# Performance work log

Measured on AMD Instinct MI355X. Metric: run time of the kernel, lower is better.

Reference implementation:

```python
import jax, jax.numpy as jnp
import numpy as np

DIM = 512

def setup_inputs() -> dict:
    key = jax.random.key(0)
    kx, kq, kk, kv = jax.random.split(key, 4)
    x = jax.random.normal(kx, (8, 2048, DIM), dtype=jnp.float32)
    # Dense kernels are [in_dim, out_dim], no bias
    Wq = jax.random.normal(kq, (DIM, DIM), dtype=jnp.float32) * (DIM ** -0.5)
    Wk = jax.random.normal(kk, (DIM, DIM), dtype=jnp.float32) * (DIM ** -0.5)
    Wv = jax.random.normal(kv, (DIM, DIM), dtype=jnp.float32) * (DIM ** -0.5)
    return {"x": x, "Wq": Wq, "Wk": Wk, "Wv": Wv}

def reference(x, Wq, Wk, Wv):
    # x: [b, s, d]
    q = jnp.einsum('bsd,de->bse', x, Wq)
    k = jnp.einsum('bsd,de->bse', x, Wk)
    v = jnp.einsum('bsd,de->bse', x, Wv)
    scale = jnp.sqrt(jnp.asarray(DIM, dtype=x.dtype))
    attn = jnp.einsum('bqe,bke->bqk', q, k) / scale  # [b, s, s]
    attn = jax.nn.softmax(attn, axis=-1)
    return jnp.einsum('bqk,bke->bqe', attn, v)  # [b, s, d]
```

## Files before the change

kernel.cpp:

```cpp
#include <hip/hip_runtime.h>
#include <stdint.h>

typedef unsigned short u16;
typedef unsigned int u32;
typedef float floatx4 __attribute__((ext_vector_type(4)));
typedef __bf16 bf16x8 __attribute__((ext_vector_type(8)));
typedef __attribute__((address_space(1))) const u32 gu32;
typedef __attribute__((address_space(3))) u32 lu32;

#define SEQ 2048
#define DIM 512
#define NBATCH 8

#if defined(__has_builtin)
#if __has_builtin(__builtin_amdgcn_cvt_pk_bf16_f32)
#define HAVE_PK_BF16 1
#endif
#endif
#ifndef HAVE_PK_BF16
#define HAVE_PK_BF16 0
#endif

__device__ __forceinline__ u16 f2bf(float f) {
#if HAVE_PK_BF16
  auto p = __builtin_amdgcn_cvt_pk_bf16_f32(f, f);
  union { decltype(p) v; u16 u[2]; } cv; cv.v = p;
  return cv.u[0];
#else
  u32 u = __float_as_uint(f);
  u += 0x7fffu + ((u >> 16) & 1u);
  return (u16)(u >> 16);
#endif
}

__device__ __forceinline__ void stage_tile64(const u16* __restrict__ g, int ld, int k0, u16* lds) {
  const int t = threadIdx.x;
  const int wave = t >> 6, lane = t & 63;
  const int rsub = lane >> 3;
  const int lg = (lane & 7) ^ rsub;
#pragma unroll
  for (int q = 0; q < 4; ++q) {
    const int chunk = wave * 4 + q;
    const int row = chunk * 8 + rsub;
    const u16* gp = g + (size_t)row * ld + k0 + lg * 8;
    u16* lp = lds + chunk * 512 + lane * 8;
    __builtin_amdgcn_global_load_lds((gu32*)gp, (lu32*)lp, 16, 0, 0);
  }
}

__device__ __forceinline__ void gemm_core(const u16* A, const u16* BT, int lda, int ldb, int kdim,
                                          u16* As, u16* Bs, floatx4 acc[4][4]) {
  const int t = threadIdx.x;
  const int wave = t >> 6, lane = t & 63;
  const int wr = (wave >> 1) * 64, wc = (wave & 1) * 64;
  const int l15 = lane & 15, quad = lane >> 4;
  const int swz = l15 & 7;
  for (int k0 = 0; k0 < kdim; k0 += 64) {
    stage_tile64(A, lda, k0, As);
    stage_tile64(BT, ldb, k0, Bs);
    __syncthreads();
#pragma unroll
    for (int ks = 0; ks < 2; ++ks) {
      const int pg = ((ks << 2) + quad) ^ swz;
      bf16x8 af[4], bfr[4];
#pragma unroll
      for (int i = 0; i < 4; ++i) {
        af[i]  = *(const bf16x8*)(As + (wr + i * 16 + l15) * 64 + pg * 8);
        bfr[i] = *(const bf16x8*)(Bs + (wc + i * 16 + l15) * 64 + pg * 8);
      }
#pragma unroll
      for (int mi = 0; mi < 4; ++mi)
#pragma unroll
        for (int ni = 0; ni < 4; ++ni)
          acc[mi][ni] = __builtin_amdgcn_mfma_f32_16x16x32_bf16(af[mi], bfr[ni], acc[mi][ni], 0, 0, 0);
    }
    __syncthreads();
  }
}

__device__ __forceinline__ void zero_acc(floatx4 acc[4][4]) {
#pragma unroll
  for (int i = 0; i < 4; ++i)
#pragma unroll
    for (int j = 0; j < 4; ++j)
      acc[i][j] = (floatx4){0.f, 0.f, 0.f, 0.f};
}

__global__ __launch_bounds__(256) void k_prep(const float* __restrict__ x,
                                              const float* __restrict__ Wq, const float* __restrict__ Wk,
                                              const float* __restrict__ Wv,
                                              u16* __restrict__ xb, u16* __restrict__ wt) {
  __shared__ float tile[64][65];
  const int t = threadIdx.x;
  if (blockIdx.x < 4096) {
    size_t i = ((size_t)blockIdx.x * 256 + t) * 8;
    float4 a = *(const float4*)(x + i);
    float4 b = *(const float4*)(x + i + 4);
    u16 o[8] = {f2bf(a.x), f2bf(a.y), f2bf(a.z), f2bf(a.w),
                f2bf(b.x), f2bf(b.y), f2bf(b.z), f2bf(b.w)};
    *(uint4*)(xb + i) = *(const uint4*)o;
    return;
  }
  const int r = blockIdx.x - 4096;
  const int sec = r >> 6, rem = r & 63;
  const int kb = (rem & 7) * 64, nb0 = (rem >> 3) * 64;
  const float* W = (sec == 0) ? Wq : (sec == 1) ? Wk : Wv;
#pragma unroll
  for (int i = 0; i < 4; ++i) {
    int kr = i * 16 + (t >> 4), nc = (t & 15) * 4;
    float4 v = *(const float4*)&W[(size_t)(kb + kr) * 512 + nb0 + nc];
    tile[kr][nc] = v.x; tile[kr][nc + 1] = v.y; tile[kr][nc + 2] = v.z; tile[kr][nc + 3] = v.w;
  }
  __syncthreads();
#pragma unroll
  for (int i = 0; i < 4; ++i) {
    int nr = i * 16 + (t >> 4), kc = (t & 15) * 4;
    u16 o[4] = {f2bf(tile[kc][nr]), f2bf(tile[kc + 1][nr]), f2bf(tile[kc + 2][nr]), f2bf(tile[kc + 3][nr])};
    *(uint2*)&wt[(size_t)(sec * 512 + nb0 + nr) * 512 + kb + kc] = *(const uint2*)o;
  }
}

__global__ __launch_bounds__(256, 4) void k_qkv(const u16* __restrict__ xb, const u16* __restrict__ wt,
                                                u16* __restrict__ qo, u16* __restrict__ ko,
                                                u16* __restrict__ vt) {
  __shared__ __align__(16) u16 As[128 * 64];
  __shared__ __align__(16) u16 Bs[128 * 64];
  const int m0 = blockIdx.x * 128, n0 = blockIdx.y * 128;
  floatx4 acc[4][4];
  zero_acc(acc);
  gemm_core(xb + (size_t)m0 * DIM, wt + (size_t)n0 * DIM, DIM, DIM, DIM, As, Bs, acc);
  const int t = threadIdx.x, wave = t >> 6, lane = t & 63;
  const int wr = (wave >> 1) * 64, wc = (wave & 1) * 64;
  const int l15 = lane & 15, quad = lane >> 4;
  const int sec = n0 >> 9;
#pragma unroll
  for (int mi = 0; mi < 4; ++mi)
#pragma unroll
    for (int ni = 0; ni < 4; ++ni)
#pragma unroll
      for (int r = 0; r < 4; ++r) {
        int m = m0 + wr + mi * 16 + quad * 4 + r;
        int n = n0 + wc + ni * 16 + l15;
        float v = acc[mi][ni][r];
        int nc = n & 511;
        if (sec == 0) {
          qo[(size_t)m * DIM + nc] = f2bf(v * 0.04419417382415922f);
        } else if (sec == 1) {
          ko[(size_t)m * DIM + nc] = f2bf(v);
        } else {
          int b = m >> 11, s = m & 2047;
          vt[((size_t)(b * DIM + nc)) * SEQ + s] = f2bf(v);
        }
      }
}

__global__ __launch_bounds__(256, 4) void k_scores(const u16* __restrict__ q, const u16* __restrict__ kk,
                                                   u16* __restrict__ sc, float* __restrict__ rowsum,
                                                   int b0) {
  __shared__ __align__(16) u16 As[128 * 64];
  __shared__ __align__(16) u16 Bs[128 * 64];
  const int bz = blockIdx.z, bb = b0 + bz;
  const int xcd = blockIdx.x & 7, j = blockIdx.x >> 3;
  const int m0 = (j & 15) * 128, n0 = (xcd * 2 + (j >> 4)) * 128;
  floatx4 acc[4][4];
  zero_acc(acc);
  gemm_core(q + (size_t)bb * SEQ * DIM + (size_t)m0 * DIM,
            kk + (size_t)bb * SEQ * DIM + (size_t)n0 * DIM, DIM, DIM, DIM, As, Bs, acc);
  u16* C = sc + (size_t)bz * SEQ * SEQ;
  float* rsb = rowsum + (size_t)bb * SEQ;
  const int t = threadIdx.x, wave = t >> 6, lane = t & 63;
  const int wr = (wave >> 1) * 64, wc = (wave & 1) * 64;
  const int l15 = lane & 15, quad = lane >> 4;
#pragma unroll
  for (int mi = 0; mi < 4; ++mi)
#pragma unroll
    for (int r = 0; r < 4; ++r) {
      int m = m0 + wr + mi * 16 + quad * 4 + r;
      float p = 0.f;
      float ev[4];
#pragma unroll
      for (int ni = 0; ni < 4; ++ni) {
        ev[ni] = __expf(acc[mi][ni][r]);
        p += ev[ni];
      }
#pragma unroll
      for (int ni = 0; ni < 4; ++ni) {
        int n = n0 + wc + ni * 16 + l15;
        C[(size_t)m * SEQ + n] = f2bf(ev[ni]);
      }
      p += __shfl_xor(p, 1); p += __shfl_xor(p, 2);
      p += __shfl_xor(p, 4); p += __shfl_xor(p, 8);
      if (l15 == 0) atomicAdd(&rsb[m], p);
    }
}

__global__ __launch_bounds__(256, 4) void k_pv(const u16* __restrict__ sc, const u16* __restrict__ vt,
                                               const float* __restrict__ rowsum,
                                               float* __restrict__ out, int b0) {
  __shared__ __align__(16) u16 As[128 * 64];
  __shared__ __align__(16) u16 Bs[128 * 64];
  const int bz = blockIdx.z, bb = b0 + bz;
  const int xcd = blockIdx.x & 7, j = blockIdx.x >> 3;
  const int m0 = (xcd * 2 + (j & 1)) * 128, n0 = (j >> 1) * 128;
  floatx4 acc[4][4];
  zero_acc(acc);
  gemm_core(sc + (size_t)bz * SEQ * SEQ + (size_t)m0 * SEQ,
            vt + (size_t)bb * DIM * SEQ + (size_t)n0 * SEQ, SEQ, SEQ, SEQ, As, Bs, acc);
  float* C = out + (size_t)bb * SEQ * DIM;
  const float* rsb = rowsum + (size_t)bb * SEQ;
  const int t = threadIdx.x, wave = t >> 6, lane = t & 63;
  const int wr = (wave >> 1) * 64, wc = (wave & 1) * 64;
  const int l15 = lane & 15, quad = lane >> 4;
#pragma unroll
  for (int mi = 0; mi < 4; ++mi)
#pragma unroll
    for (int r = 0; r < 4; ++r) {
      int m = m0 + wr + mi * 16 + quad * 4 + r;
      float inv = 1.0f / rsb[m];
#pragma unroll
      for (int ni = 0; ni < 4; ++ni) {
        int n = n0 + wc + ni * 16 + l15;
        C[(size_t)m * DIM + n] = acc[mi][ni][r] * inv;
      }
    }
}

extern "C" void kernel_launch(void* const* d_in, const int* in_sizes, int n_in,
                              void* d_out, int out_size, void* d_ws, size_t ws_size,
                              hipStream_t stream) {
  const float* x  = (const float*)d_in[0];
  const float* Wq = (const float*)d_in[1];
  const float* Wk = (const float*)d_in[2];
  const float* Wv = (const float*)d_in[3];
  float* out = (float*)d_out;
  char* ws = (char*)d_ws;

  u16* xb   = (u16*)(ws + 0);
  u16* wt   = (u16*)(ws + 16777216);
  u16* qo   = (u16*)(ws + 18350080);
  u16* ko   = (u16*)(ws + 35127296);
  u16* vt   = (u16*)(ws + 51904512);
  float* rs = (float*)(ws + 68681728);
  u16* sc   = (u16*)(ws + 68747264);
  const size_t base_need = 68747264;
  const size_t per_b = (size_t)SEQ * SEQ * 2;
  size_t avail = (ws_size > base_need) ? (ws_size - base_need) : 0;
  int nb = (int)(avail / per_b);
  if (nb < 1) nb = 1;
  if (nb > NBATCH) nb = NBATCH;

  hipMemsetAsync(rs, 0, (size_t)NBATCH * SEQ * sizeof(float), stream);
  k_prep<<<dim3(4288), dim3(256), 0, stream>>>(x, Wq, Wk, Wv, xb, wt);
  k_qkv<<<dim3(128, 12), dim3(256), 0, stream>>>(xb, wt, qo, ko, vt);
  for (int b0 = 0; b0 < NBATCH; b0 += nb) {
    int nbr = (NBATCH - b0 < nb) ? (NBATCH - b0) : nb;
    k_scores<<<dim3(256, 1, nbr), dim3(256), 0, stream>>>(qo, ko, sc, rs, b0);
    k_pv<<<dim3(64, 1, nbr), dim3(256), 0, stream>>>(sc, vt, rs, out, b0);
  }
}
```

Baseline: 216.0 us.

## Replace block-shared GEMM staging with per-wave double-buffered LDS pipeline

Swaps the block-wide staged GEMM core, which needed two __syncthreads per K step, for a per-wave core. Each wave stages its own 64x32 A and B tiles into private LDS buffers, double-buffered and issued two steps ahead, and uses vmcnt waits instead of barriers. Per-block LDS rises to 64KB, so launch bounds drop to 2 blocks per CU. k_qkv is also remapped to a 1D grid with XCD-aware tile ordering. The intent is to overlap global-to-LDS loads with MFMA work and remove block barriers, at the cost of fetching shared A/B rows once per wave and lower occupancy.

```diff
diff --git a/kernel.cpp b/kernel.cpp
--- a/kernel.cpp
+++ b/kernel.cpp
@@ -12,70 +12,62 @@
 #define DIM 512
 #define NBATCH 8
 
-#if defined(__has_builtin)
-#if __has_builtin(__builtin_amdgcn_cvt_pk_bf16_f32)
-#define HAVE_PK_BF16 1
-#endif
-#endif
-#ifndef HAVE_PK_BF16
-#define HAVE_PK_BF16 0
-#endif
-
 __device__ __forceinline__ u16 f2bf(float f) {
-#if HAVE_PK_BF16
-  auto p = __builtin_amdgcn_cvt_pk_bf16_f32(f, f);
-  union { decltype(p) v; u16 u[2]; } cv; cv.v = p;
-  return cv.u[0];
-#else
   u32 u = __float_as_uint(f);
   u += 0x7fffu + ((u >> 16) & 1u);
   return (u16)(u >> 16);
-#endif
-}
-
-__device__ __forceinline__ void stage_tile64(const u16* __restrict__ g, int ld, int k0, u16* lds) {
-  const int t = threadIdx.x;
-  const int wave = t >> 6, lane = t & 63;
-  const int rsub = lane >> 3;
-  const int lg = (lane & 7) ^ rsub;
-#pragma unroll
-  for (int q = 0; q < 4; ++q) {
-    const int chunk = wave * 4 + q;
-    const int row = chunk * 8 + rsub;
-    const u16* gp = g + (size_t)row * ld + k0 + lg * 8;
-    u16* lp = lds + chunk * 512 + lane * 8;
-    __builtin_amdgcn_global_load_lds((gu32*)gp, (lu32*)lp, 16, 0, 0);
-  }
-}
-
-__device__ __forceinline__ void gemm_core(const u16* A, const u16* BT, int lda, int ldb, int kdim,
-                                          u16* As, u16* Bs, floatx4 acc[4][4]) {
-  const int t = threadIdx.x;
-  const int wave = t >> 6, lane = t & 63;
-  const int wr = (wave >> 1) * 64, wc = (wave & 1) * 64;
-  const int l15 = lane & 15, quad = lane >> 4;
-  const int swz = l15 & 7;
-  for (int k0 = 0; k0 < kdim; k0 += 64) {
-    stage_tile64(A, lda, k0, As);
-    stage_tile64(BT, ldb, k0, Bs);
-    __syncthreads();
-#pragma unroll
-    for (int ks = 0; ks < 2; ++ks) {
-      const int pg = ((ks << 2) + quad) ^ swz;
-      bf16x8 af[4], bfr[4];
-#pragma unroll
-      for (int i = 0; i < 4; ++i) {
-        af[i]  = *(const bf16x8*)(As + (wr + i * 16 + l15) * 64 + pg * 8);
-        bfr[i] = *(const bf16x8*)(Bs + (wc + i * 16 + l15) * 64 + pg * 8);
-      }
-#pragma unroll
-      for (int mi = 0; mi < 4; ++mi)
-#pragma unroll
-        for (int ni = 0; ni < 4; ++ni)
-          acc[mi][ni] = __builtin_amdgcn_mfma_f32_16x16x32_bf16(af[mi], bfr[ni], acc[mi][ni], 0, 0, 0);
-    }
-    __syncthreads();
-  }
+}
+
+template<int KDIM>
+__device__ __forceinline__ void gemm_core_p(const u16* __restrict__ Ah, const u16* __restrict__ Bh,
+                                            int lda, int ldb, u16* __restrict__ wbuf,
+                                            floatx4 acc[4][4]) {
+  const int lane = threadIdx.x & 63;
+  const int l15 = lane & 15, quad = lane >> 4;
+  const int rsub = lane >> 2;
+  const int lg = (lane & 3) ^ ((rsub >> 1) & 3);
+  constexpr int NIT = KDIM / 32;
+
+  u16* const Ab[2] = {wbuf, wbuf + 2048};
+  u16* const Bb[2] = {wbuf + 4096, wbuf + 6144};
+
+  auto stg = [&](int s, int k0) {
+#pragma unroll
+    for (int c = 0; c < 4; ++c)
+      __builtin_amdgcn_global_load_lds((gu32*)(Ah + (size_t)(c * 16 + rsub) * lda + k0 + lg * 8),
+                                       (lu32*)(Ab[s] + c * 512 + lane * 8), 16, 0, 0);
+#pragma unroll
+    for (int c = 0; c < 4; ++c)
+      __builtin_amdgcn_global_load_lds((gu32*)(Bh + (size_t)(c * 16 + rsub) * ldb + k0 + lg * 8),
+                                       (lu32*)(Bb[s] + c * 512 + lane * 8), 16, 0, 0);
+  };
+  auto body = [&](int k, int s, bool last) {
+    if (last) asm volatile("s_waitcnt vmcnt(0)" ::: "memory");
+    else      asm volatile("s_waitcnt vmcnt(8)" ::: "memory");
+    bf16x8 af[4], bf[4];
+    const int pg = quad ^ ((l15 >> 1) & 3);
+#pragma unroll
+    for (int i = 0; i < 4; ++i) {
+      af[i] = *(const bf16x8*)(Ab[s] + (i * 16 + l15) * 32 + pg * 8);
+      bf[i] = *(const bf16x8*)(Bb[s] + (i * 16 + l15) * 32 + pg * 8);
+    }
+    if (k + 2 < NIT) {
+      asm volatile("s_waitcnt lgkmcnt(0)" ::: "memory");
+      stg(s, (k + 2) * 32);
+    }
+#pragma unroll
+    for (int mi = 0; mi < 4; ++mi)
+#pragma unroll
+      for (int ni = 0; ni < 4; ++ni)
+        acc[mi][ni] = __builtin_amdgcn_mfma_f32_16x16x32_bf16(af[mi], bf[ni], acc[mi][ni], 0, 0, 0);
+  };
+
+  stg(0, 0);
+  stg(1, 32);
+#pragma unroll 2
+  for (int k = 0; k < NIT - 2; ++k) body(k, k & 1, false);
+  body(NIT - 2, (NIT - 2) & 1, false);
+  body(NIT - 1, (NIT - 1) & 1, true);
 }
 
 __device__ __forceinline__ void zero_acc(floatx4 acc[4][4]) {
@@ -120,17 +112,20 @@
   }
 }
 
-__global__ __launch_bounds__(256, 4) void k_qkv(const u16* __restrict__ xb, const u16* __restrict__ wt,
+__global__ __launch_bounds__(256, 2) void k_qkv(const u16* __restrict__ xb, const u16* __restrict__ wt,
                                                 u16* __restrict__ qo, u16* __restrict__ ko,
                                                 u16* __restrict__ vt) {
-  __shared__ __align__(16) u16 As[128 * 64];
-  __shared__ __align__(16) u16 Bs[128 * 64];
-  const int m0 = blockIdx.x * 128, n0 = blockIdx.y * 128;
+  __shared__ __align__(16) u16 SB[32768];
+  const int lid = blockIdx.x;
+  const int xcd = lid & 7, j = lid >> 3;
+  const int m0 = (xcd * 16 + (j & 15)) * 128;
+  const int n0 = (j >> 4) * 128;
+  const int t = threadIdx.x, wave = t >> 6, lane = t & 63;
+  const int wr = (wave >> 1) * 64, wc = (wave & 1) * 64;
   floatx4 acc[4][4];
   zero_acc(acc);
-  gemm_core(xb + (size_t)m0 * DIM, wt + (size_t)n0 * DIM, DIM, DIM, DIM, As, Bs, acc);
-  const int t = threadIdx.x, wave = t >> 6, lane = t & 63;
-  const int wr = (wave >> 1) * 64, wc = (wave & 1) * 64;
+  gemm_core_p<DIM>(xb + (size_t)(m0 + wr) * DIM, wt + (size_t)(n0 + wc) * DIM,
+                   DIM, DIM, SB + wave * 8192, acc);
   const int l15 = lane & 15, quad = lane >> 4;
   const int sec = n0 >> 9;
 #pragma unroll
@@ -154,22 +149,22 @@
       }
 }
 
-__global__ __launch_bounds__(256, 4) void k_scores(const u16* __restrict__ q, const u16* __restrict__ kk,
+__global__ __launch_bounds__(256, 2) void k_scores(const u16* __restrict__ q, const u16* __restrict__ kk,
                                                    u16* __restrict__ sc, float* __restrict__ rowsum,
                                                    int b0) {
-  __shared__ __align__(16) u16 As[128 * 64];
-  __shared__ __align__(16) u16 Bs[128 * 64];
+  __shared__ __align__(16) u16 SB[32768];
   const int bz = blockIdx.z, bb = b0 + bz;
   const int xcd = blockIdx.x & 7, j = blockIdx.x >> 3;
   const int m0 = (j & 15) * 128, n0 = (xcd * 2 + (j >> 4)) * 128;
+  const int t = threadIdx.x, wave = t >> 6, lane = t & 63;
+  const int wr = (wave >> 1) * 64, wc = (wave & 1) * 64;
   floatx4 acc[4][4];
   zero_acc(acc);
-  gemm_core(q + (size_t)bb * SEQ * DIM + (size_t)m0 * DIM,
-            kk + (size_t)bb * SEQ * DIM + (size_t)n0 * DIM, DIM, DIM, DIM, As, Bs, acc);
+  gemm_core_p<DIM>(q + (size_t)bb * SEQ * DIM + (size_t)(m0 + wr) * DIM,
+                   kk + (size_t)bb * SEQ * DIM + (size_t)(n0 + wc) * DIM,
+                   DIM, DIM, SB + wave * 8192, acc);
   u16* C = sc + (size_t)bz * SEQ * SEQ;
   float* rsb = rowsum + (size_t)bb * SEQ;
-  const int t = threadIdx.x, wave = t >> 6, lane = t & 63;
-  const int wr = (wave >> 1) * 64, wc = (wave & 1) * 64;
   const int l15 = lane & 15, quad = lane >> 4;
 #pragma unroll
   for (int mi = 0; mi < 4; ++mi)
@@ -194,22 +189,22 @@
     }
 }
 
-__global__ __launch_bounds__(256, 4) void k_pv(const u16* __restrict__ sc, const u16* __restrict__ vt,
+__global__ __launch_bounds__(256, 2) void k_pv(const u16* __restrict__ sc, const u16* __restrict__ vt,
                                                const float* __restrict__ rowsum,
                                                float* __restrict__ out, int b0) {
-  __shared__ __align__(16) u16 As[128 * 64];
-  __shared__ __align__(16) u16 Bs[128 * 64];
+  __shared__ __align__(16) u16 SB[32768];
   const int bz = blockIdx.z, bb = b0 + bz;
   const int xcd = blockIdx.x & 7, j = blockIdx.x >> 3;
   const int m0 = (xcd * 2 + (j & 1)) * 128, n0 = (j >> 1) * 128;
+  const int t = threadIdx.x, wave = t >> 6, lane = t & 63;
+  const int wr = (wave >> 1) * 64, wc = (wave & 1) * 64;
   floatx4 acc[4][4];
   zero_acc(acc);
-  gemm_core(sc + (size_t)bz * SEQ * SEQ + (size_t)m0 * SEQ,
-            vt + (size_t)bb * DIM * SEQ + (size_t)n0 * SEQ, SEQ, SEQ, SEQ, As, Bs, acc);
+  gemm_core_p<SEQ>(sc + (size_t)bz * SEQ * SEQ + (size_t)(m0 + wr) * SEQ,
+                   vt + (size_t)bb * DIM * SEQ + (size_t)(n0 + wc) * SEQ,
+                   SEQ, SEQ, SB + wave * 8192, acc);
   float* C = out + (size_t)bb * SEQ * DIM;
   const float* rsb = rowsum + (size_t)bb * SEQ;
-  const int t = threadIdx.x, wave = t >> 6, lane = t & 63;
-  const int wr = (wave >> 1) * 64, wc = (wave & 1) * 64;
   const int l15 = lane & 15, quad = lane >> 4;
 #pragma unroll
   for (int mi = 0; mi < 4; ++mi)
@@ -251,7 +246,7 @@
 
   hipMemsetAsync(rs, 0, (size_t)NBATCH * SEQ * sizeof(float), stream);
   k_prep<<<dim3(4288), dim3(256), 0, stream>>>(x, Wq, Wk, Wv, xb, wt);
-  k_qkv<<<dim3(128, 12), dim3(256), 0, stream>>>(xb, wt, qo, ko, vt);
+  k_qkv<<<dim3(1536), dim3(256), 0, stream>>>(xb, wt, qo, ko, vt);
   for (int b0 = 0; b0 < NBATCH; b0 += nb) {
     int nbr = (NBATCH - b0 < nb) ? (NBATCH - b0) : nb;
     k_scores<<<dim3(256, 1, nbr), dim3(256), 0, stream>>>(qo, ko, sc, rs, b0);
```

Result: slower. 267.2 us (+23.7%).
